# Kernel optimization log

Hardware: AMD Instinct MI355X
Metric: run time of the kernel (lower is better)

The kernel has to match this reference:

```python
import jax, jax.numpy as jnp
import numpy as np

B, S, H = 1, 1024, 2048
E, I, TOP_K = 64, 768, 8


def setup_inputs() -> dict:
    key = jax.random.key(0)
    k1, k2, k3, k4, k5 = jax.random.split(key, 5)
    std = 0.02
    return {
        "hidden_states": jax.random.normal(k1, (B, S, H), dtype=jnp.float32),
        "router_w": jax.random.normal(k2, (E, H), dtype=jnp.float32) * std,
        "gate_w": jax.random.normal(k3, (E, I, H), dtype=jnp.float32) * std,
        "up_w": jax.random.normal(k4, (E, I, H), dtype=jnp.float32) * std,
        "down_w": jax.random.normal(k5, (E, H, I), dtype=jnp.float32) * std,
    }


def reference(hidden_states, router_w, gate_w, up_w, down_w):
    b, s, h = hidden_states.shape
    x = hidden_states.reshape(-1, h)                     # [T, H]
    T = x.shape[0]

    # Router: softmax in fp32, top-k, renormalize (matches torch source).
    logits = x @ router_w.T                              # [T, E]
    probs = jax.nn.softmax(logits.astype(jnp.float32), axis=-1)
    topk_w, topk_idx = jax.lax.top_k(probs, TOP_K)       # [T, K]
    topk_w = topk_w / jnp.sum(topk_w, axis=-1, keepdims=True)
    topk_w = topk_w.astype(hidden_states.dtype)

    # Dense combine weights: zero for unselected experts. [T, E]
    tok = jnp.arange(T)[:, None]
    combine = jnp.zeros((T, E), dtype=hidden_states.dtype).at[tok, topk_idx].add(topk_w)

    # Scan over experts: SwiGLU MLP on all tokens, weighted-accumulate.
    # Tokens with zero combine weight contribute nothing (same math as the
    # gather/scatter loop in the torch source).
    def body(acc, p):
        gw, uw, dw, cw = p                                # [I,H],[I,H],[H,I],[T]
        hidden = jax.nn.silu(x @ gw.T) * (x @ uw.T)       # [T, I]
        out = hidden @ dw.T                               # [T, H]
        return acc + cw[:, None] * out, None

    init = jnp.zeros_like(x)
    final, _ = jax.lax.scan(body, init, (gate_w, up_w, down_w, combine.T))
    return final.reshape(b, s, h)
```

## Files before the change

### kernel.cpp

```cpp
#include <hip/hip_runtime.h>

#define T_TOK 1024
#define HD    2048
#define NE    64
#define ID    768
#define TOPK  8

typedef __bf16 bf16x8 __attribute__((ext_vector_type(8)));
typedef float  f32x4  __attribute__((ext_vector_type(4)));

__device__ __forceinline__ void load_lds16(const void* src, void* lds) {
  __builtin_amdgcn_global_load_lds(
      (__attribute__((address_space(1))) const void*)src,
      (__attribute__((address_space(3))) void*)lds, 16, 0, 0);
}

__global__ __launch_bounds__(256) void router_kernel(
    const float* __restrict__ x, const float* __restrict__ rw,
    unsigned short* __restrict__ xb_u, float* __restrict__ tw,
    int* __restrict__ counts, int* __restrict__ lists)
{
  __shared__ float  sx[HD];
  __shared__ double slog[NE];
  const int t = blockIdx.x;
  const int tid = threadIdx.x;
  __bf16* xb = (__bf16*)xb_u;

  for (int i = tid; i < HD; i += 256) {
    float v = x[(size_t)t * HD + i];
    sx[i] = v;
    xb[(size_t)t * HD + i] = (__bf16)v;
  }
  __syncthreads();

  const int e = tid >> 2, p = tid & 3;
  const float* rwrow = rw + (size_t)e * HD;
  double acc = 0.0;
  for (int k = p; k < HD; k += 4)
    acc += (double)sx[k] * (double)rwrow[k];
  acc += __shfl_xor(acc, 1, 64);
  acc += __shfl_xor(acc, 2, 64);
  if (p == 0) slog[e] = acc;
  __syncthreads();

  if (tid < 64) {
    double v = slog[tid];
    double selv = -1e300; int seli = 0; double gmax = 0.0;
    #pragma unroll
    for (int k = 0; k < TOPK; ++k) {
      double bv = v; int bi = tid;
      #pragma unroll
      for (int off = 32; off >= 1; off >>= 1) {
        double ov = __shfl_xor(bv, off, 64);
        int    oi = __shfl_xor(bi, off, 64);
        if (ov > bv || (ov == bv && oi < bi)) { bv = ov; bi = oi; }
      }
      if (k == 0) gmax = bv;
      if (tid == k) { selv = bv; seli = bi; }
      if (tid == bi) v = -1e300;
    }
    double e_ = (tid < TOPK) ? exp(selv - gmax) : 0.0;
    double s = e_;
    #pragma unroll
    for (int off = 32; off >= 1; off >>= 1) s += __shfl_xor(s, off, 64);
    if (tid < TOPK) {
      int slot = t * TOPK + tid;
      tw[slot] = (float)(e_ / s);
      int pos = atomicAdd(&counts[seli], 1);
      lists[seli * T_TOK + pos] = slot;
    }
  }
}

__global__ __launch_bounds__(256, 2) void gemm1_kernel(
    const unsigned short* __restrict__ xb_u,
    const float* __restrict__ gw, const float* __restrict__ uw,
    const int* __restrict__ counts, const int* __restrict__ lists,
    const unsigned short* __restrict__ zp_u,
    unsigned short* __restrict__ hb_u)
{
  __shared__ __bf16 sA[256 * 64];
  __shared__ __bf16 sG[64 * 64];
  __shared__ __bf16 sU[64 * 64];
  __shared__ int    sSlot[256];

  const __bf16* xb = (const __bf16*)xb_u;
  const __bf16* zp = (const __bf16*)zp_u;
  __bf16* hb = (__bf16*)hb_u;

  const int e   = blockIdx.y;
  const int n0  = blockIdx.x * 64;
  const int tid = threadIdx.x;
  const int wid = tid >> 6;
  const int lane = tid & 63;
  const int n_e = counts[e];

  for (int m0 = 0; m0 < n_e; m0 += 256) {
    sSlot[tid] = (m0 + tid < n_e) ? lists[e * T_TOK + m0 + tid] : -1;
    __syncthreads();

    const __bf16* abase[8];
    #pragma unroll
    for (int i = 0; i < 8; ++i) {
      int r = wid * 64 + i * 8 + (lane >> 3);
      int slot = sSlot[r];
      int sl = (lane & 7) ^ (r & 7);
      abase[i] = (slot >= 0) ? (xb + (size_t)(slot >> 3) * HD + sl * 8)
                             : (zp + sl * 8);
    }

    f32x4 accg[4][4], accu[4][4];
    const f32x4 vzero = {0.f, 0.f, 0.f, 0.f};
    #pragma unroll
    for (int r = 0; r < 4; ++r)
      #pragma unroll
      for (int c = 0; c < 4; ++c) { accg[r][c] = vzero; accu[r][c] = vzero; }

    const int rows_here = n_e - m0 - wid * 64;

    for (int kt = 0; kt < HD / 64; ++kt) {
      const int k0 = kt * 64;
      #pragma unroll
      for (int i = 0; i < 8; ++i)
        load_lds16(abase[i] + k0, &sA[(wid * 8 + i) * 512]);

      #pragma unroll
      for (int i = 0; i < 2; ++i) {
        int c = i * 256 + tid;
        int row = c >> 3, sl = c & 7;
        size_t boff = ((size_t)e * ID + n0 + row) * HD + (size_t)(k0 + sl * 8);
        f32x4 g0 = *(const f32x4*)(gw + boff);
        f32x4 g1 = *(const f32x4*)(gw + boff + 4);
        f32x4 u0 = *(const f32x4*)(uw + boff);
        f32x4 u1 = *(const f32x4*)(uw + boff + 4);
        bf16x8 gb, ub;
        #pragma unroll
        for (int j = 0; j < 4; ++j) {
          gb[j] = (__bf16)g0[j]; gb[j + 4] = (__bf16)g1[j];
          ub[j] = (__bf16)u0[j]; ub[j + 4] = (__bf16)u1[j];
        }
        int ph = sl ^ (row & 7);
        *(bf16x8*)&sG[row * 64 + ph * 8] = gb;
        *(bf16x8*)&sU[row * 64 + ph * 8] = ub;
      }
      __syncthreads();

      #pragma unroll
      for (int kk = 0; kk < 2; ++kk) {
        bf16x8 aF[4];
        #pragma unroll
        for (int r = 0; r < 4; ++r) if (r * 16 < rows_here) {
          int row = wid * 64 + r * 16 + (lane & 15);
          int ph = (kk * 4 + (lane >> 4)) ^ (row & 7);
          aF[r] = *(const bf16x8*)&sA[row * 64 + ph * 8];
        }
        #pragma unroll
        for (int c = 0; c < 4; ++c) {
          int row = c * 16 + (lane & 15);
          int ph = (kk * 4 + (lane >> 4)) ^ (row & 7);
          bf16x8 gF = *(const bf16x8*)&sG[row * 64 + ph * 8];
          bf16x8 uF = *(const bf16x8*)&sU[row * 64 + ph * 8];
          #pragma unroll
          for (int r = 0; r < 4; ++r) if (r * 16 < rows_here) {
            accg[r][c] = __builtin_amdgcn_mfma_f32_16x16x32_bf16(aF[r], gF, accg[r][c], 0, 0, 0);
            accu[r][c] = __builtin_amdgcn_mfma_f32_16x16x32_bf16(aF[r], uF, accu[r][c], 0, 0, 0);
          }
        }
      }
      __syncthreads();
    }

    #pragma unroll
    for (int r = 0; r < 4; ++r) if (r * 16 < rows_here) {
      #pragma unroll
      for (int j = 0; j < 4; ++j) {
        int row = wid * 64 + r * 16 + (lane >> 4) * 4 + j;
        if (m0 + row < n_e) {
          int slot = sSlot[row];
          #pragma unroll
          for (int c = 0; c < 4; ++c) {
            float g = accg[r][c][j], u = accu[r][c][j];
            float h = (g / (1.0f + expf(-g))) * u;
            hb[(size_t)slot * ID + (size_t)(n0 + c * 16 + (lane & 15))] = (__bf16)h;
          }
        }
      }
    }
    __syncthreads();
  }
}

__global__ __launch_bounds__(256, 2) void gemm2_kernel(
    const unsigned short* __restrict__ hb_u,
    const float* __restrict__ dw,
    const int* __restrict__ counts, const int* __restrict__ lists,
    const float* __restrict__ tw,
    const unsigned short* __restrict__ zp_u,
    float* __restrict__ out)
{
  __shared__ __bf16 sA[256 * 64];
  __shared__ __bf16 sB[64 * 64];
  __shared__ int    sSlot[256];

  const __bf16* hbuf = (const __bf16*)hb_u;
  const __bf16* zp   = (const __bf16*)zp_u;

  const int e   = blockIdx.y;
  const int n0  = blockIdx.x * 64;
  const int tid = threadIdx.x;
  const int wid = tid >> 6;
  const int lane = tid & 63;
  const int n_e = counts[e];

  for (int m0 = 0; m0 < n_e; m0 += 256) {
    sSlot[tid] = (m0 + tid < n_e) ? lists[e * T_TOK + m0 + tid] : -1;
    __syncthreads();

    const __bf16* abase[8];
    #pragma unroll
    for (int i = 0; i < 8; ++i) {
      int r = wid * 64 + i * 8 + (lane >> 3);
      int slot = sSlot[r];
      int sl = (lane & 7) ^ (r & 7);
      abase[i] = (slot >= 0) ? (hbuf + (size_t)slot * ID + sl * 8)
                             : (zp + sl * 8);
    }

    f32x4 acc[4][4];
    const f32x4 vzero = {0.f, 0.f, 0.f, 0.f};
    #pragma unroll
    for (int r = 0; r < 4; ++r)
      #pragma unroll
      for (int c = 0; c < 4; ++c) acc[r][c] = vzero;

    const int rows_here = n_e - m0 - wid * 64;

    for (int kt = 0; kt < ID / 64; ++kt) {
      const int k0 = kt * 64;
      #pragma unroll
      for (int i = 0; i < 8; ++i)
        load_lds16(abase[i] + k0, &sA[(wid * 8 + i) * 512]);

      #pragma unroll
      for (int i = 0; i < 2; ++i) {
        int c = i * 256 + tid;
        int row = c >> 3, sl = c & 7;
        size_t boff = ((size_t)e * HD + n0 + row) * ID + (size_t)(k0 + sl * 8);
        f32x4 b0 = *(const f32x4*)(dw + boff);
        f32x4 b1 = *(const f32x4*)(dw + boff + 4);
        bf16x8 bb;
        #pragma unroll
        for (int j = 0; j < 4; ++j) { bb[j] = (__bf16)b0[j]; bb[j + 4] = (__bf16)b1[j]; }
        int ph = sl ^ (row & 7);
        *(bf16x8*)&sB[row * 64 + ph * 8] = bb;
      }
      __syncthreads();

      #pragma unroll
      for (int kk = 0; kk < 2; ++kk) {
        bf16x8 aF[4];
        #pragma unroll
        for (int r = 0; r < 4; ++r) if (r * 16 < rows_here) {
          int row = wid * 64 + r * 16 + (lane & 15);
          int ph = (kk * 4 + (lane >> 4)) ^ (row & 7);
          aF[r] = *(const bf16x8*)&sA[row * 64 + ph * 8];
        }
        #pragma unroll
        for (int c = 0; c < 4; ++c) {
          int row = c * 16 + (lane & 15);
          int ph = (kk * 4 + (lane >> 4)) ^ (row & 7);
          bf16x8 bF = *(const bf16x8*)&sB[row * 64 + ph * 8];
          #pragma unroll
          for (int r = 0; r < 4; ++r) if (r * 16 < rows_here) {
            acc[r][c] = __builtin_amdgcn_mfma_f32_16x16x32_bf16(aF[r], bF, acc[r][c], 0, 0, 0);
          }
        }
      }
      __syncthreads();
    }

    #pragma unroll
    for (int r = 0; r < 4; ++r) if (r * 16 < rows_here) {
      #pragma unroll
      for (int j = 0; j < 4; ++j) {
        int row = wid * 64 + r * 16 + (lane >> 4) * 4 + j;
        if (m0 + row < n_e) {
          int slot = sSlot[row];
          int token = slot >> 3;
          float w = tw[slot];
          #pragma unroll
          for (int c = 0; c < 4; ++c) {
            atomicAdd(out + (size_t)token * HD + (size_t)(n0 + c * 16 + (lane & 15)),
                      w * acc[r][c][j]);
          }
        }
      }
    }
    __syncthreads();
  }
}

extern "C" void kernel_launch(void* const* d_in, const int* in_sizes, int n_in,
                              void* d_out, int out_size, void* d_ws, size_t ws_size,
                              hipStream_t stream) {
  const float* x  = (const float*)d_in[0];
  const float* rw = (const float*)d_in[1];
  const float* gw = (const float*)d_in[2];
  const float* uw = (const float*)d_in[3];
  const float* dw = (const float*)d_in[4];
  float* out = (float*)d_out;

  char* ws = (char*)d_ws;
  const size_t ZP_OFF  = 0;
  const size_t XB_OFF  = 8192;
  const size_t TW_OFF  = XB_OFF + (size_t)T_TOK * HD * 2;
  const size_t CNT_OFF = TW_OFF + (size_t)T_TOK * TOPK * 4;
  const size_t LST_OFF = CNT_OFF + 256;
  const size_t HB_OFF  = LST_OFF + (size_t)NE * T_TOK * 4;

  unsigned short* zp  = (unsigned short*)(ws + ZP_OFF);
  unsigned short* xb  = (unsigned short*)(ws + XB_OFF);
  float*          tw  = (float*)(ws + TW_OFF);
  int*            cnt = (int*)(ws + CNT_OFF);
  int*            lst = (int*)(ws + LST_OFF);
  unsigned short* hb  = (unsigned short*)(ws + HB_OFF);

  hipMemsetAsync(zp, 0, 8192, stream);
  hipMemsetAsync(cnt, 0, 256, stream);
  hipMemsetAsync(d_out, 0, (size_t)T_TOK * HD * sizeof(float), stream);

  router_kernel<<<T_TOK, 256, 0, stream>>>(x, rw, xb, tw, cnt, lst);
  gemm1_kernel<<<dim3(ID / 64, NE), 256, 0, stream>>>(xb, gw, uw, cnt, lst, zp, hb);
  gemm2_kernel<<<dim3(HD / 64, NE), 256, 0, stream>>>(hb, dw, cnt, lst, tw, zp, out);
}
```

Baseline: 520.4 us.

## Double-buffer MoE GEMM tiles with 512-thread blocks and XCD-aware block remapping

Both expert GEMM kernels now use 512-thread workgroups of eight waves, each wave owning 32 rows, and K-tiles of 32 held in double-buffered LDS. The next tile's activations (async global-to-LDS) and fp32 weights (into registers) are prefetched while the current tile is computed, and each step needs one barrier instead of two. The grid is flattened and remapped so that blocks working on the same expert land on the same XCD, which should improve L2 reuse of weights. The trade is more barriers per unit of K, since the tiles are half as deep, and more register and LDS pressure from the launch bounds of 512 threads with four blocks per CU.

```diff
diff --git a/kernel.cpp b/kernel.cpp
--- a/kernel.cpp
+++ b/kernel.cpp
@@ -7,11 +7,12 @@
 #define TOPK  8
 
 typedef __bf16 bf16x8 __attribute__((ext_vector_type(8)));
+typedef __bf16 bf16x4 __attribute__((ext_vector_type(4)));
 typedef float  f32x4  __attribute__((ext_vector_type(4)));
 
 __device__ __forceinline__ void load_lds16(const void* src, void* lds) {
   __builtin_amdgcn_global_load_lds(
-      (__attribute__((address_space(1))) const void*)src,
+      (const __attribute__((address_space(1))) void*)src,
       (__attribute__((address_space(3))) void*)lds, 16, 0, 0);
 }
 
@@ -72,109 +73,112 @@
   }
 }
 
-__global__ __launch_bounds__(256, 2) void gemm1_kernel(
+__global__ __launch_bounds__(512, 4) void gemm1_kernel(
     const unsigned short* __restrict__ xb_u,
     const float* __restrict__ gw, const float* __restrict__ uw,
     const int* __restrict__ counts, const int* __restrict__ lists,
     const unsigned short* __restrict__ zp_u,
     unsigned short* __restrict__ hb_u)
 {
-  __shared__ __bf16 sA[256 * 64];
-  __shared__ __bf16 sG[64 * 64];
-  __shared__ __bf16 sU[64 * 64];
+  __shared__ __bf16 sA[2][256 * 32];
+  __shared__ __bf16 sG[2][64 * 32];
+  __shared__ __bf16 sU[2][64 * 32];
   __shared__ int    sSlot[256];
 
   const __bf16* xb = (const __bf16*)xb_u;
   const __bf16* zp = (const __bf16*)zp_u;
   __bf16* hb = (__bf16*)hb_u;
 
-  const int e   = blockIdx.y;
-  const int n0  = blockIdx.x * 64;
-  const int tid = threadIdx.x;
-  const int wid = tid >> 6;
+  const int wg  = blockIdx.x;
+  const int idx = wg >> 3;
+  const int e   = (wg & 7) * 8 + idx / 12;
+  const int n0  = (idx % 12) * 64;
+
+  const int tid  = threadIdx.x;
+  const int wid  = tid >> 6;
   const int lane = tid & 63;
-  const int n_e = counts[e];
+  const int n_e  = counts[e];
+
+  const int wrow = tid >> 3;
+  const int wqc  = tid & 7;
+  const size_t wsrc0 = ((size_t)e * ID + n0 + wrow) * HD + (size_t)wqc * 4;
+  const int wds = wrow * 32 + (((wqc >> 1) ^ ((wrow >> 1) & 3)) * 8) + (wqc & 1) * 4;
 
   for (int m0 = 0; m0 < n_e; m0 += 256) {
-    sSlot[tid] = (m0 + tid < n_e) ? lists[e * T_TOK + m0 + tid] : -1;
+    if (tid < 256) sSlot[tid] = (m0 + tid < n_e) ? lists[e * T_TOK + m0 + tid] : -1;
     __syncthreads();
 
-    const __bf16* abase[8];
-    #pragma unroll
-    for (int i = 0; i < 8; ++i) {
-      int r = wid * 64 + i * 8 + (lane >> 3);
+    const __bf16* abase[2];
+    #pragma unroll
+    for (int j = 0; j < 2; ++j) {
+      int r = wid * 32 + j * 16 + (lane >> 2);
       int slot = sSlot[r];
-      int sl = (lane & 7) ^ (r & 7);
-      abase[i] = (slot >= 0) ? (xb + (size_t)(slot >> 3) * HD + sl * 8)
-                             : (zp + sl * 8);
-    }
-
-    f32x4 accg[4][4], accu[4][4];
+      int cs = (lane & 3) ^ ((r >> 1) & 3);
+      abase[j] = (slot >= 0) ? (xb + (size_t)(slot >> 3) * HD + cs * 8)
+                             : (zp + cs * 8);
+    }
+
+    f32x4 accg[2][4], accu[2][4];
     const f32x4 vzero = {0.f, 0.f, 0.f, 0.f};
     #pragma unroll
-    for (int r = 0; r < 4; ++r)
+    for (int r = 0; r < 2; ++r)
       #pragma unroll
       for (int c = 0; c < 4; ++c) { accg[r][c] = vzero; accu[r][c] = vzero; }
 
-    const int rows_here = n_e - m0 - wid * 64;
-
-    for (int kt = 0; kt < HD / 64; ++kt) {
-      const int k0 = kt * 64;
-      #pragma unroll
-      for (int i = 0; i < 8; ++i)
-        load_lds16(abase[i] + k0, &sA[(wid * 8 + i) * 512]);
-
-      #pragma unroll
-      for (int i = 0; i < 2; ++i) {
-        int c = i * 256 + tid;
-        int row = c >> 3, sl = c & 7;
-        size_t boff = ((size_t)e * ID + n0 + row) * HD + (size_t)(k0 + sl * 8);
-        f32x4 g0 = *(const f32x4*)(gw + boff);
-        f32x4 g1 = *(const f32x4*)(gw + boff + 4);
-        f32x4 u0 = *(const f32x4*)(uw + boff);
-        f32x4 u1 = *(const f32x4*)(uw + boff + 4);
-        bf16x8 gb, ub;
-        #pragma unroll
-        for (int j = 0; j < 4; ++j) {
-          gb[j] = (__bf16)g0[j]; gb[j + 4] = (__bf16)g1[j];
-          ub[j] = (__bf16)u0[j]; ub[j + 4] = (__bf16)u1[j];
-        }
-        int ph = sl ^ (row & 7);
-        *(bf16x8*)&sG[row * 64 + ph * 8] = gb;
-        *(bf16x8*)&sU[row * 64 + ph * 8] = ub;
-      }
-      __syncthreads();
-
-      #pragma unroll
-      for (int kk = 0; kk < 2; ++kk) {
-        bf16x8 aF[4];
-        #pragma unroll
-        for (int r = 0; r < 4; ++r) if (r * 16 < rows_here) {
-          int row = wid * 64 + r * 16 + (lane & 15);
-          int ph = (kk * 4 + (lane >> 4)) ^ (row & 7);
-          aF[r] = *(const bf16x8*)&sA[row * 64 + ph * 8];
-        }
-        #pragma unroll
-        for (int c = 0; c < 4; ++c) {
-          int row = c * 16 + (lane & 15);
-          int ph = (kk * 4 + (lane >> 4)) ^ (row & 7);
-          bf16x8 gF = *(const bf16x8*)&sG[row * 64 + ph * 8];
-          bf16x8 uF = *(const bf16x8*)&sU[row * 64 + ph * 8];
-          #pragma unroll
-          for (int r = 0; r < 4; ++r) if (r * 16 < rows_here) {
-            accg[r][c] = __builtin_amdgcn_mfma_f32_16x16x32_bf16(aF[r], gF, accg[r][c], 0, 0, 0);
-            accu[r][c] = __builtin_amdgcn_mfma_f32_16x16x32_bf16(aF[r], uF, accu[r][c], 0, 0, 0);
-          }
-        }
-      }
-      __syncthreads();
-    }
-
-    #pragma unroll
-    for (int r = 0; r < 4; ++r) if (r * 16 < rows_here) {
+    const int rows_here = n_e - m0 - wid * 32;
+
+    #pragma unroll
+    for (int j = 0; j < 2; ++j)
+      load_lds16(abase[j], &sA[0][(wid * 32 + j * 16) * 32]);
+    f32x4 ga = *(const f32x4*)(gw + wsrc0);
+    f32x4 ua = *(const f32x4*)(uw + wsrc0);
+    f32x4 gb_, ub_;
+
+#define G1_STEP(KT, BC, BN_, GC, UC, GN, UN)                                      \
+    {                                                                             \
+      bf16x4 gv, uv;                                                              \
+      _Pragma("unroll") for (int q = 0; q < 4; ++q) {                             \
+        gv[q] = (__bf16)GC[q]; uv[q] = (__bf16)UC[q];                             \
+      }                                                                           \
+      *(bf16x4*)&sG[BC][wds] = gv;                                                \
+      *(bf16x4*)&sU[BC][wds] = uv;                                                \
+      __syncthreads();                                                            \
+      if ((KT) + 1 < HD / 32) {                                                   \
+        const int k1 = ((KT) + 1) * 32;                                           \
+        _Pragma("unroll") for (int j = 0; j < 2; ++j)                             \
+          load_lds16(abase[j] + k1, &sA[BN_][(wid * 32 + j * 16) * 32]);          \
+        GN = *(const f32x4*)(gw + wsrc0 + (size_t)k1);                            \
+        UN = *(const f32x4*)(uw + wsrc0 + (size_t)k1);                            \
+      }                                                                           \
+      bf16x8 aF[2];                                                               \
+      _Pragma("unroll") for (int r = 0; r < 2; ++r) if (r * 16 < rows_here) {     \
+        int row = wid * 32 + r * 16 + (lane & 15);                                \
+        int ph = (lane >> 4) ^ ((row >> 1) & 3);                                  \
+        aF[r] = *(const bf16x8*)&sA[BC][row * 32 + ph * 8];                       \
+      }                                                                           \
+      _Pragma("unroll") for (int c = 0; c < 4; ++c) {                             \
+        int row = c * 16 + (lane & 15);                                           \
+        int ph = (lane >> 4) ^ ((row >> 1) & 3);                                  \
+        bf16x8 gF = *(const bf16x8*)&sG[BC][row * 32 + ph * 8];                   \
+        bf16x8 uF = *(const bf16x8*)&sU[BC][row * 32 + ph * 8];                   \
+        _Pragma("unroll") for (int r = 0; r < 2; ++r) if (r * 16 < rows_here) {   \
+          accg[r][c] = __builtin_amdgcn_mfma_f32_16x16x32_bf16(aF[r], gF, accg[r][c], 0, 0, 0); \
+          accu[r][c] = __builtin_amdgcn_mfma_f32_16x16x32_bf16(aF[r], uF, accu[r][c], 0, 0, 0); \
+        }                                                                         \
+      }                                                                           \
+    }
+
+    for (int it = 0; it < (HD / 32) / 2; ++it) {
+      G1_STEP(2 * it,     0, 1, ga,  ua,  gb_, ub_);
+      G1_STEP(2 * it + 1, 1, 0, gb_, ub_, ga,  ua);
+    }
+#undef G1_STEP
+
+    #pragma unroll
+    for (int r = 0; r < 2; ++r) if (r * 16 < rows_here) {
       #pragma unroll
       for (int j = 0; j < 4; ++j) {
-        int row = wid * 64 + r * 16 + (lane >> 4) * 4 + j;
+        int row = wid * 32 + r * 16 + (lane >> 4) * 4 + j;
         if (m0 + row < n_e) {
           int slot = sSlot[row];
           #pragma unroll
@@ -190,7 +194,7 @@
   }
 }
 
-__global__ __launch_bounds__(256, 2) void gemm2_kernel(
+__global__ __launch_bounds__(512, 4) void gemm2_kernel(
     const unsigned short* __restrict__ hb_u,
     const float* __restrict__ dw,
     const int* __restrict__ counts, const int* __restrict__ lists,
@@ -198,92 +202,96 @@
     const unsigned short* __restrict__ zp_u,
     float* __restrict__ out)
 {
-  __shared__ __bf16 sA[256 * 64];
-  __shared__ __bf16 sB[64 * 64];
+  __shared__ __bf16 sA[2][256 * 32];
+  __shared__ __bf16 sB[2][64 * 32];
   __shared__ int    sSlot[256];
 
   const __bf16* hbuf = (const __bf16*)hb_u;
   const __bf16* zp   = (const __bf16*)zp_u;
 
-  const int e   = blockIdx.y;
-  const int n0  = blockIdx.x * 64;
-  const int tid = threadIdx.x;
-  const int wid = tid >> 6;
+  const int wg  = blockIdx.x;
+  const int idx = wg >> 3;
+  const int e   = (wg & 7) * 8 + idx / 32;
+  const int n0  = (idx % 32) * 64;
+
+  const int tid  = threadIdx.x;
+  const int wid  = tid >> 6;
   const int lane = tid & 63;
-  const int n_e = counts[e];
+  const int n_e  = counts[e];
+
+  const int wrow = tid >> 3;
+  const int wqc  = tid & 7;
+  const size_t wsrc0 = ((size_t)e * HD + n0 + wrow) * ID + (size_t)wqc * 4;
+  const int wds = wrow * 32 + (((wqc >> 1) ^ ((wrow >> 1) & 3)) * 8) + (wqc & 1) * 4;
 
   for (int m0 = 0; m0 < n_e; m0 += 256) {
-    sSlot[tid] = (m0 + tid < n_e) ? lists[e * T_TOK + m0 + tid] : -1;
+    if (tid < 256) sSlot[tid] = (m0 + tid < n_e) ? lists[e * T_TOK + m0 + tid] : -1;
     __syncthreads();
 
-    const __bf16* abase[8];
-    #pragma unroll
-    for (int i = 0; i < 8; ++i) {
-      int r = wid * 64 + i * 8 + (lane >> 3);
+    const __bf16* abase[2];
+    #pragma unroll
+    for (int j = 0; j < 2; ++j) {
+      int r = wid * 32 + j * 16 + (lane >> 2);
       int slot = sSlot[r];
-      int sl = (lane & 7) ^ (r & 7);
-      abase[i] = (slot >= 0) ? (hbuf + (size_t)slot * ID + sl * 8)
-                             : (zp + sl * 8);
-    }
-
-    f32x4 acc[4][4];
+      int cs = (lane & 3) ^ ((r >> 1) & 3);
+      abase[j] = (slot >= 0) ? (hbuf + (size_t)slot * ID + cs * 8)
+                             : (zp + cs * 8);
+    }
+
+    f32x4 acc[2][4];
     const f32x4 vzero = {0.f, 0.f, 0.f, 0.f};
     #pragma unroll
-    for (int r = 0; r < 4; ++r)
+    for (int r = 0; r < 2; ++r)
       #pragma unroll
       for (int c = 0; c < 4; ++c) acc[r][c] = vzero;
 
-    const int rows_here = n_e - m0 - wid * 64;
-
-    for (int kt = 0; kt < ID / 64; ++kt) {
-      const int k0 = kt * 64;
-      #pragma unroll
-      for (int i = 0; i < 8; ++i)
-        load_lds16(abase[i] + k0, &sA[(wid * 8 + i) * 512]);
-
-      #pragma unroll
-      for (int i = 0; i < 2; ++i) {
-        int c = i * 256 + tid;
-        int row = c >> 3, sl = c & 7;
-        size_t boff = ((size_t)e * HD + n0 + row) * ID + (size_t)(k0 + sl * 8);
-        f32x4 b0 = *(const f32x4*)(dw + boff);
-        f32x4 b1 = *(const f32x4*)(dw + boff + 4);
-        bf16x8 bb;
-        #pragma unroll
-        for (int j = 0; j < 4; ++j) { bb[j] = (__bf16)b0[j]; bb[j + 4] = (__bf16)b1[j]; }
-        int ph = sl ^ (row & 7);
-        *(bf16x8*)&sB[row * 64 + ph * 8] = bb;
-      }
-      __syncthreads();
-
-      #pragma unroll
-      for (int kk = 0; kk < 2; ++kk) {
-        bf16x8 aF[4];
-        #pragma unroll
-        for (int r = 0; r < 4; ++r) if (r * 16 < rows_here) {
-          int row = wid * 64 + r * 16 + (lane & 15);
-          int ph = (kk * 4 + (lane >> 4)) ^ (row & 7);
-          aF[r] = *(const bf16x8*)&sA[row * 64 + ph * 8];
-        }
-        #pragma unroll
-        for (int c = 0; c < 4; ++c) {
-          int row = c * 16 + (lane & 15);
-          int ph = (kk * 4 + (lane >> 4)) ^ (row & 7);
-          bf16x8 bF = *(const bf16x8*)&sB[row * 64 + ph * 8];
-          #pragma unroll
-          for (int r = 0; r < 4; ++r) if (r * 16 < rows_here) {
-            acc[r][c] = __builtin_amdgcn_mfma_f32_16x16x32_bf16(aF[r], bF, acc[r][c], 0, 0, 0);
-          }
-        }
-      }
-      __syncthreads();
-    }
-
-    #pragma unroll
-    for (int r = 0; r < 4; ++r) if (r * 16 < rows_here) {
+    const int rows_here = n_e - m0 - wid * 32;
+
+    #pragma unroll
+    for (int j = 0; j < 2; ++j)
+      load_lds16(abase[j], &sA[0][(wid * 32 + j * 16) * 32]);
+    f32x4 da = *(const f32x4*)(dw + wsrc0);
+    f32x4 db_;
+
+#define G2_STEP(KT, BC, BN_, DC, DN)                                              \
+    {                                                                             \
+      bf16x4 dv;                                                                  \
+      _Pragma("unroll") for (int q = 0; q < 4; ++q) dv[q] = (__bf16)DC[q];        \
+      *(bf16x4*)&sB[BC][wds] = dv;                                                \
+      __syncthreads();                                                            \
+      if ((KT) + 1 < ID / 32) {                                                   \
+        const int k1 = ((KT) + 1) * 32;                                           \
+        _Pragma("unroll") for (int j = 0; j < 2; ++j)                             \
+          load_lds16(abase[j] + k1, &sA[BN_][(wid * 32 + j * 16) * 32]);          \
+        DN = *(const f32x4*)(dw + wsrc0 + (size_t)k1);                            \
+      }                                                                           \
+      bf16x8 aF[2];                                                               \
+      _Pragma("unroll") for (int r = 0; r < 2; ++r) if (r * 16 < rows_here) {     \
+        int row = wid * 32 + r * 16 + (lane & 15);                                \
+        int ph = (lane >> 4) ^ ((row >> 1) & 3);                                  \
+        aF[r] = *(const bf16x8*)&sA[BC][row * 32 + ph * 8];                       \
+      }                                                                           \
+      _Pragma("unroll") for (int c = 0; c < 4; ++c) {                             \
+        int row = c * 16 + (lane & 15);                                           \
+        int ph = (lane >> 4) ^ ((row >> 1) & 3);                                  \
+        bf16x8 bF = *(const bf16x8*)&sB[BC][row * 32 + ph * 8];                   \
+        _Pragma("unroll") for (int r = 0; r < 2; ++r) if (r * 16 < rows_here) {   \
+          acc[r][c] = __builtin_amdgcn_mfma_f32_16x16x32_bf16(aF[r], bF, acc[r][c], 0, 0, 0); \
+        }                                                                         \
+      }                                                                           \
+    }
+
+    for (int it = 0; it < (ID / 32) / 2; ++it) {
+      G2_STEP(2 * it,     0, 1, da,  db_);
+      G2_STEP(2 * it + 1, 1, 0, db_, da);
+    }
+#undef G2_STEP
+
+    #pragma unroll
+    for (int r = 0; r < 2; ++r) if (r * 16 < rows_here) {
       #pragma unroll
       for (int j = 0; j < 4; ++j) {
-        int row = wid * 64 + r * 16 + (lane >> 4) * 4 + j;
+        int row = wid * 32 + r * 16 + (lane >> 4) * 4 + j;
         if (m0 + row < n_e) {
           int slot = sSlot[row];
           int token = slot >> 3;
@@ -330,6 +338,6 @@
   hipMemsetAsync(d_out, 0, (size_t)T_TOK * HD * sizeof(float), stream);
 
   router_kernel<<<T_TOK, 256, 0, stream>>>(x, rw, xb, tw, cnt, lst);
-  gemm1_kernel<<<dim3(ID / 64, NE), 256, 0, stream>>>(xb, gw, uw, cnt, lst, zp, hb);
-  gemm2_kernel<<<dim3(HD / 64, NE), 256, 0, stream>>>(hb, dw, cnt, lst, tw, zp, out);
-}
+  gemm1_kernel<<<768, 512, 0, stream>>>(xb, gw, uw, cnt, lst, zp, hb);
+  gemm2_kernel<<<2048, 512, 0, stream>>>(hb, dw, cnt, lst, tw, zp, out);
+}
```

Result: faster. 504.7 us (-3.0%).
